# Kernel tuning notes

Measured on AMD Instinct MI355X. Metric: run time of the kernel, lower is better.

The kernel has to match this reference:

```python
import jax, jax.numpy as jnp
import numpy as np

EPS = 1e-4

def setup_inputs() -> dict:
    key = jax.random.key(0)
    k1, k2, k3 = jax.random.split(key, 3)
    batch, keysize, dict_size, categories = 4096, 512, 16384, 100
    x = jax.random.normal(k1, (batch, keysize), dtype=jnp.float32)
    keys = jax.random.normal(k2, (dict_size, keysize), dtype=jnp.float32) * 0.1  # TruncatedNormal(0, 0.1) approx
    values = jax.random.uniform(k3, (dict_size, categories), dtype=jnp.float32)
    return {"x": x, "keys": keys, "values": values}


def reference(x, keys, values):
    # sq_distance(keys, x): (dict_size, batch)
    kk = jnp.sum(keys * keys, axis=1)[:, None]          # (D, 1)
    xx = jnp.sum(x * x, axis=1)[None, :]                # (1, B)
    d = kk - 2.0 * jnp.matmul(keys, x.T) + xx           # (D, B)
    kern = 1.0 / (d + EPS)                              # reciprocal kernel
    # transpose -> (B, D), matmul values (D, C) -> (B, C)
    return jnp.matmul(kern.T, values)
```

## Files before the change

kernel.cpp:

```cpp
#include <hip/hip_runtime.h>
#include <hip/hip_bf16.h>
#include <hip/hip_fp8.h>
#include <cstdint>


#define BSZ   4096
#define DSZ   16384
#define KSZ   512
#define CC    100
#define CP    128
#define EPSV  1e-4f

#define BM     64
#define BD     64
#define DSPLIT 8
#define DCHUNK (DSZ / DSPLIT)
#define NITER  (DCHUNK / BD)
#define KTS    72

typedef short  short8 __attribute__((ext_vector_type(8)));
typedef float  f32x4  __attribute__((ext_vector_type(4)));
typedef long   lng2   __attribute__((ext_vector_type(2)));
typedef unsigned int   u32;
typedef unsigned short u16;
typedef unsigned char  u8;

__device__ __forceinline__ u16 f2bf(float f) {
    union { float f; u32 u; } cv; cv.f = f;
    u32 u = cv.u;
    u += 0x7fffu + ((u >> 16) & 1u);
    return (u16)(u >> 16);
}
__device__ __forceinline__ u32 pack2(float a, float b) {
    return (u32)f2bf(a) | ((u32)f2bf(b) << 16);
}
__device__ __forceinline__ u8 f2fp8(float f) {
    __hip_fp8_e4m3 t(f);
    return *reinterpret_cast<u8*>(&t);
}

__device__ __forceinline__ void gload_lds16(const void* g, void* l) {
    __builtin_amdgcn_global_load_lds(
        (const __attribute__((address_space(1))) u32*)g,
        (__attribute__((address_space(3))) u32*)l, 16, 0, 0);
}

#define XK_BLOCKS ((DSZ + BSZ) / 4)
#define V_BLOCKS  ((CP * DSZ / 8) / 256)

__global__ __launch_bounds__(256)
void convert_all(const float* __restrict__ x, const float* __restrict__ keys,
                 const float* __restrict__ values,
                 u8* __restrict__ xw, u8* __restrict__ kw, u16* __restrict__ vw,
                 float* __restrict__ kk, float* __restrict__ xx)
{
    const int tid = threadIdx.x;
    if (blockIdx.x < XK_BLOCKS) {
        const int wid = tid >> 6, lane = tid & 63;
        const int row = blockIdx.x * 4 + wid;
        const float* src; u8* dst; float* nrm; int r;
        if (row < DSZ) { r = row;       src = keys + (size_t)r * KSZ; dst = kw + (size_t)r * KSZ; nrm = kk + r; }
        else           { r = row - DSZ; src = x    + (size_t)r * KSZ; dst = xw + (size_t)r * KSZ; nrm = xx + r; }

        float4 v0 = *reinterpret_cast<const float4*>(src + lane * 8);
        float4 v1 = *reinterpret_cast<const float4*>(src + lane * 8 + 4);
        float s = v0.x*v0.x + v0.y*v0.y + v0.z*v0.z + v0.w*v0.w
                + v1.x*v1.x + v1.y*v1.y + v1.z*v1.z + v1.w*v1.w;

        unsigned long long pk = 0;
        pk |= (unsigned long long)f2fp8(v0.x);
        pk |= (unsigned long long)f2fp8(v0.y) << 8;
        pk |= (unsigned long long)f2fp8(v0.z) << 16;
        pk |= (unsigned long long)f2fp8(v0.w) << 24;
        pk |= (unsigned long long)f2fp8(v1.x) << 32;
        pk |= (unsigned long long)f2fp8(v1.y) << 40;
        pk |= (unsigned long long)f2fp8(v1.z) << 48;
        pk |= (unsigned long long)f2fp8(v1.w) << 56;

        const int j = lane >> 2, hi_l = lane & 3;
        const int ch = j >> 3, jl = j & 7, jj = jl >> 1, f = jl & 1;
        const int off = ch * 256 + (((jj * 64 + hi_l * 16)) ^ ((r & 7) << 4)) + f * 8;
        *reinterpret_cast<unsigned long long*>(dst + off) = pk;

        s += __shfl_xor(s, 1);  s += __shfl_xor(s, 2);  s += __shfl_xor(s, 4);
        s += __shfl_xor(s, 8);  s += __shfl_xor(s, 16); s += __shfl_xor(s, 32);
        if (lane == 0) *nrm = s;
    } else {
        const int gid = (blockIdx.x - XK_BLOCKS) * 256 + tid;
        const int c = gid >> 11;
        const int j = gid & 2047;
        const int dp  = ((j >> 3) << 6) + ((j & 7) << 3);
        const int dsg = ((j >> 3) << 6) + (((j & 7) ^ (c & 7)) << 3);
        uint4 w = make_uint4(0, 0, 0, 0);
        if (c < CC) {
            float f[8];
#pragma unroll
            for (int i = 0; i < 8; ++i) f[i] = values[(size_t)(dsg + i) * CC + c];
            w.x = pack2(f[0], f[1]); w.y = pack2(f[2], f[3]);
            w.z = pack2(f[4], f[5]); w.w = pack2(f[6], f[7]);
        }
        *reinterpret_cast<uint4*>(vw + (size_t)c * DSZ + dp) = w;
    }
}

__global__ __launch_bounds__(512, 4)
void varkeys_fast(const u8* __restrict__ xw, const u8* __restrict__ kw,
                  const u16* __restrict__ vw, const float* __restrict__ kkp,
                  const float* __restrict__ xxp, float* __restrict__ out)
{
    __shared__ __align__(16) u8  ksb0[BD * 256];
    __shared__ __align__(16) u8  ksb1[BD * 256];
    __shared__ __align__(16) u16 kT[BM * KTS];
    __shared__ __align__(16) u16 vT[CP * BD];

    const int tid  = threadIdx.x;
    const int wid  = tid >> 6;
    const int lane = tid & 63;
    const int lo   = lane & 15;
    const int hi   = lane >> 4;
    const int wm   = wid >> 1;
    const int wn   = wid & 1;

    const int h  = blockIdx.x;
    const int by = h & 7, bx = h >> 3;
    const int bm0   = bx * BM;
    const int dbase = by * DCHUNK;

    lng2 xq[8];
    {
        const int row = bm0 + wm * 16 + lo;
        const u8* base = xw + (size_t)row * KSZ;
        const int s16 = (row & 7) << 4;
#pragma unroll
        for (int ch = 0; ch < 2; ++ch)
#pragma unroll
            for (int jj = 0; jj < 4; ++jj)
                xq[ch * 4 + jj] = *reinterpret_cast<const lng2*>(
                    base + ch * 256 + ((jj * 64 + hi * 16) ^ s16));
    }
    float xr[4];
#pragma unroll
    for (int r = 0; r < 4; ++r)
        xr[r] = xxp[bm0 + wm * 16 + hi * 4 + r] + EPSV;

    f32x4 accO[4];
#pragma unroll
    for (int n = 0; n < 4; ++n) accO[n] = f32x4{0.f, 0.f, 0.f, 0.f};

#define IS_KS(BUFP, DK, CCH) { \
        _Pragma("unroll") \
        for (int i = 0; i < 2; ++i) { \
            const int ci = wid * 2 + i; \
            const int flat = ci * 1024 + lane * 16; \
            gload_lds16(kw + (size_t)((DK) + (flat >> 8)) * KSZ + (CCH) * 256 + (flat & 255), \
                        (char*)(BUFP) + ci * 1024); \
        } }

#define IS_VT(D0) { \
        _Pragma("unroll") \
        for (int i = 0; i < 2; ++i) { \
            const int ci = wid * 2 + i; \
            const int flat = ci * 512 + lane * 8; \
            gload_lds16(vw + (size_t)(flat >> 6) * DSZ + (D0) + (flat & 63), \
                        (char*)vT + ci * 1024); \
        } }

    IS_KS(ksb0, dbase, 0)
    __builtin_amdgcn_s_barrier();

    const int swz   = (lo & 7) << 3;
    const int swz16 = (lo & 7) << 4;

#define A16(CH, BUF)                                                                  \
    {                                                                                 \
        _Pragma("unroll")                                                             \
        for (int jj = 0; jj < 4; ++jj) {                                              \
            const int off = (jj * 64 + hi * 16) ^ swz16;                              \
            const u8* p0 = (const u8*)(BUF) + (wn * 32 + lo) * 256 + off;             \
            lng2 b0 = *reinterpret_cast<const lng2*>(p0);                             \
            lng2 b1 = *reinterpret_cast<const lng2*>(p0 + 16 * 256);                  \
            lng2 a0 = xq[(CH) * 4 + jj];                                              \
            accS[0] = __builtin_amdgcn_mfma_f32_16x16x32_fp8_fp8(a0[0], b0[0], accS[0], 0, 0, 0); \
            accS[1] = __builtin_amdgcn_mfma_f32_16x16x32_fp8_fp8(a0[0], b1[0], accS[1], 0, 0, 0); \
            accS[0] = __builtin_amdgcn_mfma_f32_16x16x32_fp8_fp8(a0[1], b0[1], accS[0], 0, 0, 0); \
            accS[1] = __builtin_amdgcn_mfma_f32_16x16x32_fp8_fp8(a0[1], b1[1], accS[1], 0, 0, 0); \
        }                                                                             \
    }

    for (int it = 0; it < NITER; ++it) {
        const int d0 = dbase + it * BD;

        f32x4 accS[2];
#pragma unroll
        for (int n = 0; n < 2; ++n) accS[n] = f32x4{0.f, 0.f, 0.f, 0.f};

        __builtin_amdgcn_s_barrier();
        IS_KS(ksb1, d0, 1)
        IS_VT(d0)
        const float kkf0 = kkp[d0 + wn * 32 + lo];
        const float kkf1 = kkp[d0 + wn * 32 + 16 + lo];
        asm volatile("s_waitcnt vmcnt(6)" ::: "memory");
        __builtin_amdgcn_s_barrier();
        __builtin_amdgcn_sched_barrier(0);
        A16(0, ksb0)

        __builtin_amdgcn_s_barrier();
        if (it < NITER - 1) {
            IS_KS(ksb0, d0 + BD, 0)
            asm volatile("s_waitcnt vmcnt(6)" ::: "memory");
        } else {
            asm volatile("s_waitcnt vmcnt(0)" ::: "memory");
        }
        __builtin_amdgcn_s_barrier();
        __builtin_amdgcn_sched_barrier(0);
        A16(1, ksb1)

#pragma unroll
        for (int n = 0; n < 2; ++n) {
            const int dl = wn * 32 + n * 16 + lo;
            const float kkv = n ? kkf1 : kkf0;
#pragma unroll
            for (int r = 0; r < 4; ++r) {
                const int rowl = wm * 16 + hi * 4 + r;
                const float dsq = kkv + xr[r] - 2.f * accS[n][r];
                kT[rowl * KTS + dl] = f2bf(__builtin_amdgcn_rcpf(dsq));
            }
        }
        asm volatile("s_waitcnt vmcnt(2)" ::: "memory");
        asm volatile("s_waitcnt lgkmcnt(0)" ::: "memory");
        __builtin_amdgcn_s_barrier();
        __builtin_amdgcn_sched_barrier(0);

#pragma unroll
        for (int kst = 0; kst < 2; ++kst) {
            const int k0l = kst * 32 + hi * 8;
            const int k0v = k0l ^ swz;
            short8 a0 = *reinterpret_cast<const short8*>(&kT[(wm * 16 + lo) * KTS + k0l]);
#pragma unroll
            for (int nh = 0; nh < 2; ++nh) {
                short8 b0 = *reinterpret_cast<const short8*>(&vT[(wn * 64 + nh * 32 + lo) * BD + k0v]);
                accO[nh * 2 + 0] = __builtin_amdgcn_mfma_f32_16x16x32_bf16(a0, b0, accO[nh * 2 + 0], 0, 0, 0);
                if (wn == 0 || nh == 0) {
                    short8 b1 = *reinterpret_cast<const short8*>(&vT[(wn * 64 + nh * 32 + 16 + lo) * BD + k0v]);
                    accO[nh * 2 + 1] = __builtin_amdgcn_mfma_f32_16x16x32_bf16(a0, b1, accO[nh * 2 + 1], 0, 0, 0);
                }
            }
        }
    }

#pragma unroll
    for (int n = 0; n < 4; ++n) {
        const int c = wn * 64 + n * 16 + lo;
        if (c < CC) {
#pragma unroll
            for (int r = 0; r < 4; ++r) {
                const int b_ = bm0 + wm * 16 + hi * 4 + r;
                atomicAdd(&out[(size_t)b_ * CC + c], accO[n][r]);
            }
        }
    }
#undef IS_KS
#undef IS_VT
#undef A16
}


#define FBM 128
#define XS_STRIDE 72
#define KS_STRIDE 72
#define KT_STRIDE 72
#define VL_STRIDE 106
#define FKC 64
#define FNKC (KSZ / FKC)
#define FDSPLIT 8
#define FDCHUNK (DSZ / FDSPLIT)
#define FNITER  (FDCHUNK / BD)

__global__ __launch_bounds__(256)
void varkeys_pre(const float* __restrict__ x, const float* __restrict__ keys,
                 float* __restrict__ kk, float* __restrict__ xx)
{
    const int tid  = threadIdx.x;
    const int wid  = tid >> 6;
    const int lane = tid & 63;
    const int lo   = lane & 15;
    const int sub  = lane >> 4;
    const int row  = blockIdx.x * 16 + wid * 4 + sub;
    const float* src = (row < DSZ) ? keys + (size_t)row * KSZ
                                   : x + (size_t)(row - DSZ) * KSZ;
    float s = 0.f;
#pragma unroll
    for (int j = 0; j < 8; ++j) {
        float4 v = *reinterpret_cast<const float4*>(src + j * 64 + lo * 4);
        s += v.x * v.x + v.y * v.y + v.z * v.z + v.w * v.w;
    }
    s += __shfl_xor(s, 1); s += __shfl_xor(s, 2);
    s += __shfl_xor(s, 4); s += __shfl_xor(s, 8);
    if (lo == 0) {
        if (row < DSZ) kk[row] = s;
        else           xx[row - DSZ] = s;
    }
}

__global__ __launch_bounds__(256, 2)
void varkeys_main(const float* __restrict__ x, const float* __restrict__ keys,
                  const float* __restrict__ values, float* __restrict__ out,
                  const float* __restrict__ kk_ws, const float* __restrict__ xx_ws,
                  int use_ws)
{
    __shared__ __align__(16) u16 xs[FBM * XS_STRIDE];
    __shared__ __align__(16) u16 ks[BD * KS_STRIDE];
    __shared__ __align__(16) u16 kTf[FBM * KT_STRIDE];
    __shared__ __align__(16) u16 vls[BD * VL_STRIDE];
    __shared__ float kk_s[FDCHUNK];
    __shared__ float xx_s[FBM];

    const int tid  = threadIdx.x;
    const int wid  = tid >> 6;
    const int lane = tid & 63;
    const int lo   = lane & 15;
    const int hi   = lane >> 4;
    const int wm   = wid >> 1;
    const int wn   = wid & 1;
    const int bm0   = blockIdx.x * FBM;
    const int dbase = blockIdx.y * FDCHUNK;

    if (use_ws) {
        for (int i = tid; i < FDCHUNK; i += 256) kk_s[i] = kk_ws[dbase + i];
        if (tid < FBM) xx_s[tid] = xx_ws[bm0 + tid];
    } else {
        for (int rbase = wid * 4; rbase < FDCHUNK + FBM; rbase += 16) {
            const int row = rbase + hi;
            const float* src = (row < FDCHUNK)
                ? keys + (size_t)(dbase + row) * KSZ
                : x + (size_t)(bm0 + row - FDCHUNK) * KSZ;
            float s = 0.f;
#pragma unroll
            for (int j = 0; j < 8; ++j) {
                float4 v = *reinterpret_cast<const float4*>(src + j * 64 + lo * 4);
                s += v.x * v.x + v.y * v.y + v.z * v.z + v.w * v.w;
            }
            s += __shfl_xor(s, 1); s += __shfl_xor(s, 2);
            s += __shfl_xor(s, 4); s += __shfl_xor(s, 8);
            if (lo == 0) {
                if (row < FDCHUNK) kk_s[row] = s;
                else               xx_s[row - FDCHUNK] = s;
            }
        }
    }
    __syncthreads();

    f32x4 accO[4][4];
#pragma unroll
    for (int m = 0; m < 4; ++m)
#pragma unroll
        for (int n = 0; n < 4; ++n) accO[m][n] = f32x4{0.f, 0.f, 0.f, 0.f};

    for (int it = 0; it < FNITER; ++it) {
        const int d0 = dbase + it * BD;

        f32x4 accS[4][2];
#pragma unroll
        for (int m = 0; m < 4; ++m)
#pragma unroll
            for (int n = 0; n < 2; ++n) accS[m][n] = f32x4{0.f, 0.f, 0.f, 0.f};

        for (int kc = 0; kc < FNKC; ++kc) {
            __syncthreads();
#pragma unroll
            for (int j = 0; j < 8; ++j) {
                const int idx = tid + j * 256;
                const int row = idx >> 4, c4 = idx & 15;
                float4 v = *reinterpret_cast<const float4*>(
                    x + (size_t)(bm0 + row) * KSZ + kc * FKC + c4 * 4);
                u32* dst = reinterpret_cast<u32*>(&xs[row * XS_STRIDE + c4 * 4]);
                dst[0] = pack2(v.x, v.y); dst[1] = pack2(v.z, v.w);
            }
#pragma unroll
            for (int j = 0; j < 4; ++j) {
                const int idx = tid + j * 256;
                const int row = idx >> 4, c4 = idx & 15;
                float4 v = *reinterpret_cast<const float4*>(
                    keys + (size_t)(d0 + row) * KSZ + kc * FKC + c4 * 4);
                u32* dst = reinterpret_cast<u32*>(&ks[row * KS_STRIDE + c4 * 4]);
                dst[0] = pack2(v.x, v.y); dst[1] = pack2(v.z, v.w);
            }
            __syncthreads();
#pragma unroll
            for (int kst = 0; kst < 2; ++kst) {
                const int k0 = kst * 32 + hi * 8;
                short8 a[4], b[2];
#pragma unroll
                for (int m = 0; m < 4; ++m)
                    a[m] = *reinterpret_cast<const short8*>(
                        &xs[(wm * 64 + m * 16 + lo) * XS_STRIDE + k0]);
#pragma unroll
                for (int n = 0; n < 2; ++n)
                    b[n] = *reinterpret_cast<const short8*>(
                        &ks[(wn * 32 + n * 16 + lo) * KS_STRIDE + k0]);
#pragma unroll
                for (int m = 0; m < 4; ++m)
#pragma unroll
                    for (int n = 0; n < 2; ++n)
                        accS[m][n] = __builtin_amdgcn_mfma_f32_16x16x32_bf16(
                            a[m], b[n], accS[m][n], 0, 0, 0);
            }
        }

#pragma unroll
        for (int m = 0; m < 4; ++m)
#pragma unroll
            for (int n = 0; n < 2; ++n) {
                const int dl = wn * 32 + n * 16 + lo;
                const float kkv = kk_s[it * BD + dl];
#pragma unroll
                for (int r = 0; r < 4; ++r) {
                    const int bl = wm * 64 + m * 16 + hi * 4 + r;
                    const float dsq = kkv + xx_s[bl] - 2.f * accS[m][n][r] + EPSV;
                    kTf[bl * KT_STRIDE + dl] = f2bf(__builtin_amdgcn_rcpf(dsq));
                }
            }

#pragma unroll
        for (int j = 0; j < 7; ++j) {
            const int idx = tid + j * 256;
            if (idx < 1600) {
                const int row = idx / 25, c4 = idx % 25;
                float4 v = *reinterpret_cast<const float4*>(
                    values + (size_t)(d0 + row) * CC + c4 * 4);
                u32* dst = reinterpret_cast<u32*>(&vls[row * VL_STRIDE + c4 * 4]);
                dst[0] = pack2(v.x, v.y); dst[1] = pack2(v.z, v.w);
            }
        }
        __syncthreads();

#pragma unroll
        for (int ks2 = 0; ks2 < 2; ++ks2) {
            const int k0 = ks2 * 32 + hi * 8;
            short8 a[4], b[4];
#pragma unroll
            for (int m = 0; m < 4; ++m)
                a[m] = *reinterpret_cast<const short8*>(
                    &kTf[(wm * 64 + m * 16 + lo) * KT_STRIDE + k0]);
#pragma unroll
            for (int n = 0; n < 4; ++n) {
                const int c = wn * 64 + n * 16 + lo;
                short8 t = {0, 0, 0, 0, 0, 0, 0, 0};
                if (c < CC) {
#pragma unroll
                    for (int i = 0; i < 8; ++i)
                        t[i] = (short)vls[(k0 + i) * VL_STRIDE + c];
                }
                b[n] = t;
            }
#pragma unroll
            for (int m = 0; m < 4; ++m)
#pragma unroll
                for (int n = 0; n < 4; ++n)
                    accO[m][n] = __builtin_amdgcn_mfma_f32_16x16x32_bf16(
                        a[m], b[n], accO[m][n], 0, 0, 0);
        }
    }

#pragma unroll
    for (int m = 0; m < 4; ++m)
#pragma unroll
        for (int n = 0; n < 4; ++n) {
            const int c = wn * 64 + n * 16 + lo;
            if (c < CC) {
#pragma unroll
                for (int r = 0; r < 4; ++r) {
                    const int b_ = bm0 + wm * 64 + m * 16 + hi * 4 + r;
                    atomicAdd(&out[(size_t)b_ * CC + c], accO[m][n][r]);
                }
            }
        }
}

extern "C" void kernel_launch(void* const* d_in, const int* in_sizes, int n_in,
                              void* d_out, int out_size, void* d_ws, size_t ws_size,
                              hipStream_t stream) {
    const float* x      = (const float*)d_in[0];
    const float* keys   = (const float*)d_in[1];
    const float* values = (const float*)d_in[2];
    float* out = (float*)d_out;

    hipMemsetAsync(d_out, 0, (size_t)out_size * sizeof(float), stream);

    const size_t off_xw = 0;
    const size_t off_kw = off_xw + (size_t)BSZ * KSZ;
    const size_t off_vw = off_kw + (size_t)DSZ * KSZ;
    const size_t off_kk = off_vw + (size_t)CP * DSZ * 2;
    const size_t off_xx = off_kk + (size_t)DSZ * 4;
    const size_t need   = off_xx + (size_t)BSZ * 4;

    if (ws_size >= need) {
        u8*  xw = (u8*)((char*)d_ws + off_xw);
        u8*  kw = (u8*)((char*)d_ws + off_kw);
        u16* vw = (u16*)((char*)d_ws + off_vw);
        float* kk = (float*)((char*)d_ws + off_kk);
        float* xx = (float*)((char*)d_ws + off_xx);
        convert_all<<<dim3(XK_BLOCKS + V_BLOCKS), dim3(256), 0, stream>>>(
            x, keys, values, xw, kw, vw, kk, xx);
        varkeys_fast<<<dim3(DSPLIT * (BSZ / BM)), dim3(512), 0, stream>>>(xw, kw, vw, kk, xx, out);
    } else {
        const size_t ws_need = (size_t)(DSZ + BSZ) * sizeof(float);
        const int use_ws = (ws_size >= ws_need) ? 1 : 0;
        float* kk = (float*)d_ws;
        float* xx = kk + DSZ;
        if (use_ws) {
            varkeys_pre<<<dim3((DSZ + BSZ) / 16), dim3(256), 0, stream>>>(x, keys, kk, xx);
        }
        varkeys_main<<<dim3(BSZ / FBM, FDSPLIT), dim3(256), 0, stream>>>(
            x, keys, values, out, kk, xx, use_ws);
    }
}
```

Before: 112.2 us.

## Pre-swizzle values into MFMA fragment layout and load B operands directly to registers

The conversion kernel now writes the bf16 values matrix in the exact per-lane MFMA B-fragment order, so the main kernel can load each B fragment straight from global memory into registers. This removes the vT LDS buffer, the LDS staging loads for values, and the LDS reads in the second GEMM, which frees shared memory and LDS bandwidth. The vmcnt waits are retuned for the extra outstanding global loads, and the initial barrier is dropped. The cost is more register pressure, since eight short8 fragments stay live across the first GEMM. Each wave also now loads every MFMA tile including padded columns, so it issues redundant MFMAs on the padding.

Measured after the change: 142.4 us. 26.9% more time.

```diff
diff --git a/kernel.cpp b/kernel.cpp
--- a/kernel.cpp
+++ b/kernel.cpp
@@ -51,7 +51,7 @@
 __global__ __launch_bounds__(256)
 void convert_all(const float* __restrict__ x, const float* __restrict__ keys,
                  const float* __restrict__ values,
-                 u8* __restrict__ xw, u8* __restrict__ kw, u16* __restrict__ vw,
+                 u8* __restrict__ xw, u8* __restrict__ kw, u8* __restrict__ vw2,
                  float* __restrict__ kk, float* __restrict__ xx)
 {
     const int tid = threadIdx.x;
@@ -86,32 +86,33 @@
         s += __shfl_xor(s, 8);  s += __shfl_xor(s, 16); s += __shfl_xor(s, 32);
         if (lane == 0) *nrm = s;
     } else {
-        const int gid = (blockIdx.x - XK_BLOCKS) * 256 + tid;
-        const int c = gid >> 11;
-        const int j = gid & 2047;
-        const int dp  = ((j >> 3) << 6) + ((j & 7) << 3);
-        const int dsg = ((j >> 3) << 6) + (((j & 7) ^ (c & 7)) << 3);
+        const int gid  = (blockIdx.x - XK_BLOCKS) * 256 + tid;
+        const int lane = gid & 63;
+        const int t    = gid >> 6;
+        const int kst = t & 1, hh = (t >> 1) & 1, nh = (t >> 2) & 1, wn = (t >> 3) & 1;
+        const int g   = t >> 4;
+        const int c   = wn * 64 + nh * 32 + hh * 16 + (lane & 15);
+        const int k0  = g * 64 + kst * 32 + (lane >> 4) * 8;
         uint4 w = make_uint4(0, 0, 0, 0);
         if (c < CC) {
             float f[8];
 #pragma unroll
-            for (int i = 0; i < 8; ++i) f[i] = values[(size_t)(dsg + i) * CC + c];
+            for (int e = 0; e < 8; ++e) f[e] = values[(size_t)(k0 + e) * CC + c];
             w.x = pack2(f[0], f[1]); w.y = pack2(f[2], f[3]);
             w.z = pack2(f[4], f[5]); w.w = pack2(f[6], f[7]);
         }
-        *reinterpret_cast<uint4*>(vw + (size_t)c * DSZ + dp) = w;
+        *reinterpret_cast<uint4*>(vw2 + (size_t)t * 1024 + lane * 16) = w;
     }
 }
 
 __global__ __launch_bounds__(512, 4)
 void varkeys_fast(const u8* __restrict__ xw, const u8* __restrict__ kw,
-                  const u16* __restrict__ vw, const float* __restrict__ kkp,
+                  const u8* __restrict__ vw2, const float* __restrict__ kkp,
                   const float* __restrict__ xxp, float* __restrict__ out)
 {
     __shared__ __align__(16) u8  ksb0[BD * 256];
     __shared__ __align__(16) u8  ksb1[BD * 256];
     __shared__ __align__(16) u16 kT[BM * KTS];
-    __shared__ __align__(16) u16 vT[CP * BD];
 
     const int tid  = threadIdx.x;
     const int wid  = tid >> 6;
@@ -156,19 +157,8 @@
                         (char*)(BUFP) + ci * 1024); \
         } }
 
-#define IS_VT(D0) { \
-        _Pragma("unroll") \
-        for (int i = 0; i < 2; ++i) { \
-            const int ci = wid * 2 + i; \
-            const int flat = ci * 512 + lane * 8; \
-            gload_lds16(vw + (size_t)(flat >> 6) * DSZ + (D0) + (flat & 63), \
-                        (char*)vT + ci * 1024); \
-        } }
-
     IS_KS(ksb0, dbase, 0)
-    __builtin_amdgcn_s_barrier();
-
-    const int swz   = (lo & 7) << 3;
+
     const int swz16 = (lo & 7) << 4;
 
 #define A16(CH, BUF)                                                                  \
@@ -189,32 +179,43 @@
 
     for (int it = 0; it < NITER; ++it) {
         const int d0 = dbase + it * BD;
+        const bool pf = (it < NITER - 1);
 
         f32x4 accS[2];
-#pragma unroll
-        for (int n = 0; n < 2; ++n) accS[n] = f32x4{0.f, 0.f, 0.f, 0.f};
-
-        __builtin_amdgcn_s_barrier();
+        accS[0] = f32x4{0.f, 0.f, 0.f, 0.f};
+        accS[1] = f32x4{0.f, 0.f, 0.f, 0.f};
+
         IS_KS(ksb1, d0, 1)
-        IS_VT(d0)
+        const u8* vbp = vw2 + (((size_t)(d0 >> 6) * 16 + wn * 8) << 10) + (size_t)lane * 16;
+        short8 vb0 = *reinterpret_cast<const short8*>(vbp + 0 * 1024);
+        short8 vb1 = *reinterpret_cast<const short8*>(vbp + 1 * 1024);
+        short8 vb2 = *reinterpret_cast<const short8*>(vbp + 2 * 1024);
+        short8 vb3 = *reinterpret_cast<const short8*>(vbp + 3 * 1024);
+        short8 vb4 = *reinterpret_cast<const short8*>(vbp + 4 * 1024);
+        short8 vb5 = *reinterpret_cast<const short8*>(vbp + 5 * 1024);
+        short8 vb6 = *reinterpret_cast<const short8*>(vbp + 6 * 1024);
+        short8 vb7 = *reinterpret_cast<const short8*>(vbp + 7 * 1024);
         const float kkf0 = kkp[d0 + wn * 32 + lo];
         const float kkf1 = kkp[d0 + wn * 32 + 16 + lo];
-        asm volatile("s_waitcnt vmcnt(6)" ::: "memory");
+        asm volatile("s_waitcnt vmcnt(12)" ::: "memory");
         __builtin_amdgcn_s_barrier();
         __builtin_amdgcn_sched_barrier(0);
         A16(0, ksb0)
 
         __builtin_amdgcn_s_barrier();
-        if (it < NITER - 1) {
+        __builtin_amdgcn_sched_barrier(0);
+        if (pf) {
             IS_KS(ksb0, d0 + BD, 0)
-            asm volatile("s_waitcnt vmcnt(6)" ::: "memory");
+            asm volatile("s_waitcnt vmcnt(12)" ::: "memory");
         } else {
-            asm volatile("s_waitcnt vmcnt(0)" ::: "memory");
+            asm volatile("s_waitcnt vmcnt(10)" ::: "memory");
         }
         __builtin_amdgcn_s_barrier();
         __builtin_amdgcn_sched_barrier(0);
         A16(1, ksb1)
 
+        if (pf) { asm volatile("s_waitcnt vmcnt(2)" ::: "memory"); }
+        else    { asm volatile("s_waitcnt vmcnt(0)" ::: "memory"); }
 #pragma unroll
         for (int n = 0; n < 2; ++n) {
             const int dl = wn * 32 + n * 16 + lo;
@@ -226,25 +227,23 @@
                 kT[rowl * KTS + dl] = f2bf(__builtin_amdgcn_rcpf(dsq));
             }
         }
-        asm volatile("s_waitcnt vmcnt(2)" ::: "memory");
         asm volatile("s_waitcnt lgkmcnt(0)" ::: "memory");
         __builtin_amdgcn_s_barrier();
         __builtin_amdgcn_sched_barrier(0);
 
-#pragma unroll
-        for (int kst = 0; kst < 2; ++kst) {
-            const int k0l = kst * 32 + hi * 8;
-            const int k0v = k0l ^ swz;
-            short8 a0 = *reinterpret_cast<const short8*>(&kT[(wm * 16 + lo) * KTS + k0l]);
-#pragma unroll
-            for (int nh = 0; nh < 2; ++nh) {
-                short8 b0 = *reinterpret_cast<const short8*>(&vT[(wn * 64 + nh * 32 + lo) * BD + k0v]);
-                accO[nh * 2 + 0] = __builtin_amdgcn_mfma_f32_16x16x32_bf16(a0, b0, accO[nh * 2 + 0], 0, 0, 0);
-                if (wn == 0 || nh == 0) {
-                    short8 b1 = *reinterpret_cast<const short8*>(&vT[(wn * 64 + nh * 32 + 16 + lo) * BD + k0v]);
-                    accO[nh * 2 + 1] = __builtin_amdgcn_mfma_f32_16x16x32_bf16(a0, b1, accO[nh * 2 + 1], 0, 0, 0);
-                }
-            }
+        {
+            const int k0a = 0 * 32 + hi * 8;
+            short8 a0 = *reinterpret_cast<const short8*>(&kT[(wm * 16 + lo) * KTS + k0a]);
+            accO[0] = __builtin_amdgcn_mfma_f32_16x16x32_bf16(a0, vb0, accO[0], 0, 0, 0);
+            accO[1] = __builtin_amdgcn_mfma_f32_16x16x32_bf16(a0, vb2, accO[1], 0, 0, 0);
+            accO[2] = __builtin_amdgcn_mfma_f32_16x16x32_bf16(a0, vb4, accO[2], 0, 0, 0);
+            accO[3] = __builtin_amdgcn_mfma_f32_16x16x32_bf16(a0, vb6, accO[3], 0, 0, 0);
+            const int k0b = 1 * 32 + hi * 8;
+            short8 a1 = *reinterpret_cast<const short8*>(&kT[(wm * 16 + lo) * KTS + k0b]);
+            accO[0] = __builtin_amdgcn_mfma_f32_16x16x32_bf16(a1, vb1, accO[0], 0, 0, 0);
+            accO[1] = __builtin_amdgcn_mfma_f32_16x16x32_bf16(a1, vb3, accO[1], 0, 0, 0);
+            accO[2] = __builtin_amdgcn_mfma_f32_16x16x32_bf16(a1, vb5, accO[2], 0, 0, 0);
+            accO[3] = __builtin_amdgcn_mfma_f32_16x16x32_bf16(a1, vb7, accO[3], 0, 0, 0);
         }
     }
 
@@ -260,7 +259,6 @@
         }
     }
 #undef IS_KS
-#undef IS_VT
 #undef A16
 }
 
@@ -495,14 +493,14 @@
     const size_t need   = off_xx + (size_t)BSZ * 4;
 
     if (ws_size >= need) {
-        u8*  xw = (u8*)((char*)d_ws + off_xw);
-        u8*  kw = (u8*)((char*)d_ws + off_kw);
-        u16* vw = (u16*)((char*)d_ws + off_vw);
+        u8*  xw  = (u8*)((char*)d_ws + off_xw);
+        u8*  kw  = (u8*)((char*)d_ws + off_kw);
+        u8*  vw2 = (u8*)((char*)d_ws + off_vw);
         float* kk = (float*)((char*)d_ws + off_kk);
         float* xx = (float*)((char*)d_ws + off_xx);
         convert_all<<<dim3(XK_BLOCKS + V_BLOCKS), dim3(256), 0, stream>>>(
-            x, keys, values, xw, kw, vw, kk, xx);
-        varkeys_fast<<<dim3(DSPLIT * (BSZ / BM)), dim3(512), 0, stream>>>(xw, kw, vw, kk, xx, out);
+            x, keys, values, xw, kw, vw2, kk, xx);
+        varkeys_fast<<<dim3(DSPLIT * (BSZ / BM)), dim3(512), 0, stream>>>(xw, kw, vw2, kk, xx, out);
     } else {
         const size_t ws_need = (size_t)(DSZ + BSZ) * sizeof(float);
         const int use_ws = (ws_size >= ws_need) ? 1 : 0;
```
